# Optimization experiments

Measured on AMD Instinct MI355X. Metric: run time of the kernel, lower is better.

Reference implementation:

```python
import jax, jax.numpy as jnp
import numpy as np

B, C, H, W = 4, 512, 48, 48
DQ = C // 8  # inter_rate = 8
N = H * W
EPS = 1e-5


def _local_mask(radius):
    r = np.arange(N) // W
    c = np.arange(N) % W
    d = np.maximum(np.abs(r[:, None] - r[None, :]), np.abs(c[:, None] - c[None, :]))
    return jnp.asarray(d <= radius)


def setup_inputs() -> dict:
    key = jax.random.key(0)
    ks = jax.random.split(key, 12)
    def nrm(k, shape, scale=0.04):
        return jax.random.normal(k, shape, dtype=jnp.float32) * scale
    zc = jnp.zeros((C,), jnp.float32)
    oc = jnp.ones((C,), jnp.float32)
    return {
        "x": jax.random.normal(ks[0], (B, C, H, W), dtype=jnp.float32),
        "Wq": nrm(ks[1], (DQ, C)), "bq": jnp.zeros((DQ,), jnp.float32),
        "Wk": nrm(ks[2], (DQ, C)), "bk": jnp.zeros((DQ,), jnp.float32),
        "Wv": nrm(ks[3], (C, C)), "bv": zc,
        "conv1_w": nrm(ks[4], (C, C, 3, 3)),
        "bn1_w": oc, "bn1_b": zc, "bn1_m": zc, "bn1_v": oc,
        "conv2_w": nrm(ks[5], (C, C, 3, 3)),
        "bn2_w": oc, "bn2_b": zc, "bn2_m": zc, "bn2_v": oc,
        "sig1_w": nrm(ks[6], (C, C)), "sig1_b": zc,
        "sig2_w": nrm(ks[7], (C, C)), "sig2_b": zc,
        "gamma": jnp.full((1,), 0.5, jnp.float32),
        "gamma1": jnp.full((1,), 0.3, jnp.float32),
        "gamma2": jnp.full((1,), 0.2, jnp.float32),
        "mask1": _local_mask(6),
        "mask2": _local_mask(12),
    }


def _masked_softmax(e, mask):
    # exp(e)*mask / sum(exp(e)*mask) == softmax with -inf outside mask
    e = e - jnp.max(e, axis=-1, keepdims=True)
    w = jnp.exp(e) * mask.astype(e.dtype)
    return w / jnp.sum(w, axis=-1, keepdims=True)


def _conv1x1(t, w, b):
    return jnp.einsum('bchw,dc->bdhw', t, w) + b[None, :, None, None]


def _conv3x3_bn_relu(t, w, g, beta, mu, var):
    y = jax.lax.conv_general_dilated(t, w, (1, 1), 'SAME',
                                     dimension_numbers=('NCHW', 'OIHW', 'NCHW'))
    scale = (g / jnp.sqrt(var + EPS))[None, :, None, None]
    y = (y - mu[None, :, None, None]) * scale + beta[None, :, None, None]
    return jax.nn.relu(y)


def _forward(x, Wq, bq, Wk, bk, Wv, bv, conv1_w, bn1_w, bn1_b, bn1_m, bn1_v,
             conv2_w, bn2_w, bn2_b, bn2_m, bn2_v, sig1_w, sig1_b, sig2_w, sig2_b,
             gamma, gamma1, gamma2, mask1, mask2):
    b, c, h, w = x.shape
    n = h * w
    q = _conv1x1(x, Wq, bq).reshape(b, -1, n)   # [B, d, N]
    k = _conv1x1(x, Wk, bk).reshape(b, -1, n)   # [B, d, N]
    energy = jnp.einsum('bdn,bdm->bnm', q, k)   # [B, N, N] (query rows)
    a0 = jax.nn.softmax(energy, axis=-1)
    a1 = _masked_softmax(energy, mask1)
    a2 = _masked_softmax(energy, mask2)
    v = _conv1x1(x, Wv, bv).reshape(b, c, n)
    # torch: bmm(value, attention.permute(0,2,1)) -> out[b,c,m] = sum_n v[b,c,n]*a[m,n]
    out0 = jnp.einsum('bcn,bmn->bcm', v, a0).reshape(b, c, h, w)
    out0 = gamma * out0 + x
    out0 = _conv3x3_bn_relu(out0, conv1_w, bn1_w, bn1_b, bn1_m, bn1_v)
    s1 = (jax.nn.sigmoid(_conv1x1(out0, sig1_w, sig1_b)) * out0).reshape(b, c, n)
    out1 = jnp.einsum('bcn,bmn->bcm', s1, a1).reshape(b, c, h, w)
    out1 = gamma1 * out1 + out0
    out1 = _conv3x3_bn_relu(out1, conv2_w, bn2_w, bn2_b, bn2_m, bn2_v)
    s2 = (jax.nn.sigmoid(_conv1x1(out1, sig2_w, sig2_b)) * out1).reshape(b, c, n)
    out2 = jnp.einsum('bcn,bmn->bcm', s2, a2).reshape(b, c, h, w)
    return gamma2 * out2 + out1


def reference(x, Wq, bq, Wk, bk, Wv, bv, conv1_w, bn1_w, bn1_b, bn1_m, bn1_v,
              conv2_w, bn2_w, bn2_b, bn2_m, bn2_v, sig1_w, sig1_b, sig2_w, sig2_b,
              gamma, gamma1, gamma2, mask1, mask2):
    return _forward(x, Wq, bq, Wk, bk, Wv, bv, conv1_w, bn1_w, bn1_b, bn1_m, bn1_v,
                    conv2_w, bn2_w, bn2_b, bn2_m, bn2_v, sig1_w, sig1_b, sig2_w, sig2_b,
                    gamma, gamma1, gamma2, mask1, mask2)
```

## Files before the change

### kernel.cpp

```cpp
#include <hip/hip_runtime.h>
#include <math.h>

#define BB 4
#define CC 512
#define HH 48
#define WW 48
#define NN 2304
#define DDQ 64
#define LDSP 72
#define PW 50
#define PROWS 2500

typedef __attribute__((ext_vector_type(4))) float f32x4;
typedef __attribute__((ext_vector_type(8))) _Float16 half8;
typedef __attribute__((ext_vector_type(4))) _Float16 half4;
typedef __attribute__((ext_vector_type(8))) short bf16x8;

__device__ __forceinline__ int imax(int a, int b) { return a > b ? a : b; }
__device__ __forceinline__ int imin(int a, int b) { return a < b ? a : b; }
__device__ __forceinline__ int prow(int m) {
    int h = m / WW, w = m - h * WW;
    return (h + 1) * PW + (w + 1);
}
__device__ __forceinline__ unsigned short f2bf(float f) {
    unsigned u = __float_as_uint(f);
    u += 0x7fffu + ((u >> 16) & 1u);
    return (unsigned short)(u >> 16);
}
__device__ __forceinline__ float bf2f(unsigned short s) {
    unsigned u = ((unsigned)s) << 16;
    return __uint_as_float(u);
}

typedef __attribute__((address_space(1))) unsigned int g_u32;
typedef __attribute__((address_space(3))) unsigned int l_u32;
__device__ __forceinline__ void gl16(const void* g, void* l) {
    __builtin_amdgcn_global_load_lds((const g_u32*)g, (l_u32*)l, 16, 0, 0);
}

#define BWAVE_IDX()                                  \
    int tid = threadIdx.x;                           \
    int wave = tid >> 6, lane = tid & 63;            \
    int wm = (wave >> 1) * 64, wn = (wave & 1) * 32; \
    int x = lane & 15, qq = lane >> 4;

__device__ __forceinline__ half8 fragld(const _Float16* T, int r, int c) {
    int kb = c ^ (r & 7);
    return *(const half8*)(T + r * 64 + kb * 8);
}
__device__ __forceinline__ bf16x8 fragld_b(const unsigned short* T, int r, int c) {
    int kb = c ^ (r & 7);
    return *(const bf16x8*)(T + r * 64 + kb * 8);
}

__device__ __forceinline__ void btile(const _Float16* As, const _Float16* Bs,
                                      f32x4 acc[4][2], int wm, int wn, int x, int qq) {
#pragma unroll
    for (int ks = 0; ks < 2; ++ks) {
        int c = ks * 4 + qq;
        half8 a0 = fragld(As, wm + x, c);
        half8 a1 = fragld(As, wm + 16 + x, c);
        half8 a2 = fragld(As, wm + 32 + x, c);
        half8 a3 = fragld(As, wm + 48 + x, c);
        half8 b0 = fragld(Bs, wn + x, c);
        half8 b1 = fragld(Bs, wn + 16 + x, c);
        acc[0][0] = __builtin_amdgcn_mfma_f32_16x16x32_f16(a0, b0, acc[0][0], 0, 0, 0);
        acc[0][1] = __builtin_amdgcn_mfma_f32_16x16x32_f16(a0, b1, acc[0][1], 0, 0, 0);
        acc[1][0] = __builtin_amdgcn_mfma_f32_16x16x32_f16(a1, b0, acc[1][0], 0, 0, 0);
        acc[1][1] = __builtin_amdgcn_mfma_f32_16x16x32_f16(a1, b1, acc[1][1], 0, 0, 0);
        acc[2][0] = __builtin_amdgcn_mfma_f32_16x16x32_f16(a2, b0, acc[2][0], 0, 0, 0);
        acc[2][1] = __builtin_amdgcn_mfma_f32_16x16x32_f16(a2, b1, acc[2][1], 0, 0, 0);
        acc[3][0] = __builtin_amdgcn_mfma_f32_16x16x32_f16(a3, b0, acc[3][0], 0, 0, 0);
        acc[3][1] = __builtin_amdgcn_mfma_f32_16x16x32_f16(a3, b1, acc[3][1], 0, 0, 0);
    }
}
__device__ __forceinline__ void btile_b(const unsigned short* As, const unsigned short* Bs,
                                        f32x4 acc[4][2], int wm, int wn, int x, int qq) {
#pragma unroll
    for (int ks = 0; ks < 2; ++ks) {
        int c = ks * 4 + qq;
        bf16x8 a0 = fragld_b(As, wm + x, c);
        bf16x8 a1 = fragld_b(As, wm + 16 + x, c);
        bf16x8 a2 = fragld_b(As, wm + 32 + x, c);
        bf16x8 a3 = fragld_b(As, wm + 48 + x, c);
        bf16x8 b0 = fragld_b(Bs, wn + x, c);
        bf16x8 b1 = fragld_b(Bs, wn + 16 + x, c);
        acc[0][0] = __builtin_amdgcn_mfma_f32_16x16x32_bf16(a0, b0, acc[0][0], 0, 0, 0);
        acc[0][1] = __builtin_amdgcn_mfma_f32_16x16x32_bf16(a0, b1, acc[0][1], 0, 0, 0);
        acc[1][0] = __builtin_amdgcn_mfma_f32_16x16x32_bf16(a1, b0, acc[1][0], 0, 0, 0);
        acc[1][1] = __builtin_amdgcn_mfma_f32_16x16x32_bf16(a1, b1, acc[1][1], 0, 0, 0);
        acc[2][0] = __builtin_amdgcn_mfma_f32_16x16x32_bf16(a2, b0, acc[2][0], 0, 0, 0);
        acc[2][1] = __builtin_amdgcn_mfma_f32_16x16x32_bf16(a2, b1, acc[2][1], 0, 0, 0);
        acc[3][0] = __builtin_amdgcn_mfma_f32_16x16x32_bf16(a3, b0, acc[3][0], 0, 0, 0);
        acc[3][1] = __builtin_amdgcn_mfma_f32_16x16x32_bf16(a3, b1, acc[3][1], 0, 0, 0);
    }
}

#define BACC_INIT()                                         \
    f32x4 zf = {0.f, 0.f, 0.f, 0.f};                        \
    f32x4 acc[4][2];                                        \
    _Pragma("unroll") for (int i_ = 0; i_ < 4; ++i_) {      \
        acc[i_][0] = zf; acc[i_][1] = zf; }

#define SLOT_A(i) int sb = (wave * 4 + (i)) * 64; int s = sb + lane; \
                  int r = s >> 3, kb = s & 7; int koff = ((kb ^ (r & 7)) << 3);
#define SLOT_B(i) int sb = (wave * 2 + (i)) * 64; int s = sb + lane; \
                  int r = s >> 3, kb = s & 7; int koff = ((kb ^ (r & 7)) << 3);

__device__ __forceinline__ void stage_rows(_Float16* dst, const _Float16* __restrict__ src,
                                           int ld, int row0, int k0, int tid) {
#pragma unroll
    for (int i = 0; i < 2; ++i) {
        int s = tid * 2 + i;
        int r = s >> 3, off = (s & 7) << 3;
        *(half8*)(dst + r * LDSP + off) =
            *(const half8*)(src + (size_t)(row0 + r) * ld + k0 + off);
    }
}
__device__ __forceinline__ void mfma_tile(const _Float16* As, const _Float16* Bs,
                                          f32x4 acc[2][2], int wm, int wn, int x, int qq) {
#pragma unroll
    for (int ks = 0; ks < 2; ++ks) {
        int kof = ks * 32 + qq * 8;
        half8 a0 = *(const half8*)(As + (wm + x) * LDSP + kof);
        half8 a1 = *(const half8*)(As + (wm + 16 + x) * LDSP + kof);
        half8 b0 = *(const half8*)(Bs + (wn + x) * LDSP + kof);
        half8 b1 = *(const half8*)(Bs + (wn + 16 + x) * LDSP + kof);
        acc[0][0] = __builtin_amdgcn_mfma_f32_16x16x32_f16(a0, b0, acc[0][0], 0, 0, 0);
        acc[0][1] = __builtin_amdgcn_mfma_f32_16x16x32_f16(a0, b1, acc[0][1], 0, 0, 0);
        acc[1][0] = __builtin_amdgcn_mfma_f32_16x16x32_f16(a1, b0, acc[1][0], 0, 0, 0);
        acc[1][1] = __builtin_amdgcn_mfma_f32_16x16x32_f16(a1, b1, acc[1][1], 0, 0, 0);
    }
}
#define WAVE_IDX()                             \
    int tid = threadIdx.x;                     \
    int wave = tid >> 6, lane = tid & 63;      \
    int wm = (wave >> 1) * 32, wn = (wave & 1) * 32; \
    int x = lane & 15, qq = lane >> 4;
#define ACC_INIT()                             \
    f32x4 zf = {0.f, 0.f, 0.f, 0.f};           \
    f32x4 acc[2][2];                           \
    acc[0][0] = zf; acc[0][1] = zf; acc[1][0] = zf; acc[1][1] = zf;

__global__ __launch_bounds__(256) void k_cast_multi(const float* __restrict__ s0,
                                                    const float* __restrict__ s1,
                                                    const float* __restrict__ s2,
                                                    _Float16* __restrict__ d0,
                                                    _Float16* __restrict__ d1,
                                                    _Float16* __restrict__ d2, int n) {
    const float* s = blockIdx.y == 0 ? s0 : (blockIdx.y == 1 ? s1 : s2);
    _Float16* d = blockIdx.y == 0 ? d0 : (blockIdx.y == 1 ? d1 : d2);
    for (int i = blockIdx.x * 256 + threadIdx.x; i < n; i += gridDim.x * 256)
        d[i] = (_Float16)s[i];
}

__global__ __launch_bounds__(256) void k_repack_conv2(const float* __restrict__ w1,
                                                      const float* __restrict__ w2,
                                                      _Float16* __restrict__ d1,
                                                      _Float16* __restrict__ d2) {
    const float* w = blockIdx.y ? w2 : w1;
    _Float16* dst = blockIdx.y ? d2 : d1;
    int i = blockIdx.x * 256 + threadIdx.x;
    if (i >= 9 * CC * CC) return;
    int r = i / (CC * CC);
    int rem = i - r * CC * CC;
    int co = rem / CC, ci = rem - (rem / CC) * CC;
    dst[i] = (_Float16)w[((size_t)co * CC + ci) * 9 + r];
}

__global__ __launch_bounds__(256) void k_transpose_x(const float* __restrict__ x,
                                                     _Float16* __restrict__ xT) {
    __shared__ float tile[32][33];
    int b = blockIdx.z;
    int c0 = blockIdx.y * 32, n0 = blockIdx.x * 32;
    int tx = threadIdx.x & 31, ty = threadIdx.x >> 5;
    const float* xb = x + (size_t)b * CC * NN;
#pragma unroll
    for (int rr = 0; rr < 32; rr += 8)
        tile[ty + rr][tx] = xb[(size_t)(c0 + ty + rr) * NN + n0 + tx];
    __syncthreads();
    _Float16* xTb = xT + (size_t)b * NN * CC;
#pragma unroll
    for (int rr = 0; rr < 32; rr += 8)
        xTb[(size_t)(n0 + ty + rr) * CC + c0 + tx] = (_Float16)tile[tx][ty + rr];
}

__global__ __launch_bounds__(256) void k_qkproj(const _Float16* __restrict__ Wq,
                                                const _Float16* __restrict__ Wk,
                                                const float* __restrict__ bq,
                                                const float* __restrict__ bk,
                                                const _Float16* __restrict__ xT,
                                                _Float16* __restrict__ qT,
                                                _Float16* __restrict__ kT) {
    __shared__ _Float16 As[64 * LDSP];
    __shared__ _Float16 Bs[64 * LDSP];
    WAVE_IDX();
    int j0 = blockIdx.x * 64, b = blockIdx.z;
    const _Float16* Wp = blockIdx.y ? Wk : Wq;
    const float* bias = blockIdx.y ? bk : bq;
    _Float16* outT = blockIdx.y ? kT : qT;
    const _Float16* xTb = xT + (size_t)b * NN * CC;
    ACC_INIT();
    for (int kc = 0; kc < CC; kc += 64) {
        stage_rows(As, Wp, CC, 0, kc, tid);
        stage_rows(Bs, xTb, CC, j0, kc, tid);
        __syncthreads();
        mfma_tile(As, Bs, acc, wm, wn, x, qq);
        __syncthreads();
    }
#pragma unroll
    for (int ms = 0; ms < 2; ++ms) {
        int R0 = wm + ms * 16 + qq * 4;
#pragma unroll
        for (int ns = 0; ns < 2; ++ns) {
            int Ccol = j0 + wn + ns * 16 + x;
            half4 t;
            t.x = (_Float16)(acc[ms][ns][0] + bias[R0 + 0]);
            t.y = (_Float16)(acc[ms][ns][1] + bias[R0 + 1]);
            t.z = (_Float16)(acc[ms][ns][2] + bias[R0 + 2]);
            t.w = (_Float16)(acc[ms][ns][3] + bias[R0 + 3]);
            *(half4*)(outT + ((size_t)b * NN + Ccol) * DDQ + R0) = t;
        }
    }
}

template <int EPI, int PAD>
__global__ __launch_bounds__(256) void k_cgemm(const _Float16* __restrict__ W,
                                               const float* __restrict__ bias,
                                               const _Float16* __restrict__ Bsrc,
                                               const float* __restrict__ gate,
                                               unsigned short* __restrict__ out) {
    __shared__ _Float16 As[128 * 64];
    __shared__ _Float16 Bs[64 * 64];
    BWAVE_IDX();
    int j0 = blockIdx.x * 64, i0 = blockIdx.y * 128, b = blockIdx.z;
    const _Float16* Bb = Bsrc + (size_t)b * (PAD ? (size_t)PROWS * CC : (size_t)NN * CC);

    const _Float16* aSrc[4]; int aOf[4];
#pragma unroll
    for (int i = 0; i < 4; ++i) {
        SLOT_A(i);
        aSrc[i] = W + (size_t)(i0 + r) * CC + koff;
        aOf[i] = sb * 8;
    }
    const _Float16* bSrc[2]; int bOf[2];
#pragma unroll
    for (int i = 0; i < 2; ++i) {
        SLOT_B(i);
        int row = PAD ? prow(j0 + r) : (j0 + r);
        bSrc[i] = Bb + (size_t)row * CC + koff;
        bOf[i] = sb * 8;
    }
    BACC_INIT();
    for (int kc = 0; kc < CC; kc += 64) {
        __syncthreads();
#pragma unroll
        for (int i = 0; i < 4; ++i) gl16(aSrc[i] + kc, As + aOf[i]);
#pragma unroll
        for (int i = 0; i < 2; ++i) gl16(bSrc[i] + kc, Bs + bOf[i]);
        __syncthreads();
        btile(As, Bs, acc, wm, wn, x, qq);
    }
#pragma unroll
    for (int mt = 0; mt < 4; ++mt) {
        int R0 = i0 + wm + mt * 16 + qq * 4;
#pragma unroll
        for (int nt = 0; nt < 2; ++nt) {
            int Ccol = j0 + wn + nt * 16 + x;
#pragma unroll
            for (int e = 0; e < 4; ++e) {
                float v = acc[mt][nt][e] + bias[R0 + e];
                size_t idx = ((size_t)b * CC + R0 + e) * NN + Ccol;
                if (EPI == 1) v = gate[idx] / (1.f + __expf(-v));
                out[idx] = f2bf(v);
            }
        }
    }
}

__global__ __launch_bounds__(256) void k_exp(const _Float16* __restrict__ qT,
                                             const _Float16* __restrict__ kT,
                                             unsigned short* __restrict__ attnB,
                                             float* __restrict__ rowsum, int rad) {
    __shared__ _Float16 qs[64 * LDSP];
    __shared__ _Float16 ks[64 * LDSP];
    __shared__ unsigned short Eh[64 * 72];
    __shared__ float psum[512];
    WAVE_IDX();
    int j0 = blockIdx.x * 64, i0 = blockIdx.y * 64, b = blockIdx.z;
    if (rad > 0) {
        int hlo = i0 / WW, hhi = (i0 + 63) / WW;
        int h2lo = imax(0, hlo - rad), h2hi = imin(HH - 1, hhi + rad);
        int klo = (h2lo * WW) & ~63;
        int khi = imin(NN, ((h2hi + 1) * WW + 63) & ~63);
        if (j0 + 64 <= klo || j0 >= khi) return;
    }
    stage_rows(qs, qT + (size_t)b * NN * DDQ, DDQ, i0, 0, tid);
    stage_rows(ks, kT + (size_t)b * NN * DDQ, DDQ, j0, 0, tid);
    __syncthreads();
    ACC_INIT();
    mfma_tile(qs, ks, acc, wm, wn, x, qq);
#pragma unroll
    for (int ns = 0; ns < 2; ++ns) {
        int col = wn + ns * 16 + x;
        int gn = j0 + col;
        int hn = gn / WW, cn = gn % WW;
#pragma unroll
        for (int ms = 0; ms < 2; ++ms)
#pragma unroll
            for (int e = 0; e < 4; ++e) {
                int row = wm + ms * 16 + qq * 4 + e;
                int gm = i0 + row;
                bool valid = true;
                if (rad > 0) {
                    int dh = gm / WW - hn; if (dh < 0) dh = -dh;
                    int dc = gm % WW - cn; if (dc < 0) dc = -dc;
                    valid = (dh <= rad) && (dc <= rad);
                }
                float w = valid ? __expf(acc[ms][ns][e]) : 0.f;
                Eh[row * 72 + col] = f2bf(w);
            }
    }
    __syncthreads();
#pragma unroll
    for (int t = 0; t < 2; ++t) {
        int s = tid + t * 256;
        int r = s >> 3, cg = (s & 7) << 3;
        bf16x8 v = *(const bf16x8*)(Eh + r * 72 + cg);
        *(bf16x8*)(attnB + ((size_t)b * NN + i0 + r) * NN + j0 + cg) = v;
        float ss = 0.f;
#pragma unroll
        for (int j = 0; j < 8; ++j) ss += bf2f((unsigned short)v[j]);
        psum[s] = ss;
    }
    __syncthreads();
    if (tid < 64) {
        float tot = 0.f;
#pragma unroll
        for (int g = 0; g < 8; ++g) tot += psum[tid * 8 + g];
        atomicAdd(rowsum + (size_t)b * NN + i0 + tid, tot);
    }
}

__global__ __launch_bounds__(256) void k_attn(const unsigned short* __restrict__ A,
                                              const unsigned short* __restrict__ attnB,
                                              const float* __restrict__ rowsum,
                                              const float* __restrict__ res,
                                              const float* __restrict__ gamma,
                                              float* __restrict__ outF,
                                              _Float16* __restrict__ outT, int rad) {
    __shared__ unsigned short As[128 * 64];
    __shared__ unsigned short Bs[64 * 64];
    BWAVE_IDX();
    int j0 = blockIdx.x * 64, i0 = blockIdx.y * 128, b = blockIdx.z;
    int klo = 0, khi = NN;
    if (rad > 0) {
        int hlo = j0 / WW, hhi = (j0 + 63) / WW;
        int h2lo = imax(0, hlo - rad), h2hi = imin(HH - 1, hhi + rad);
        klo = (h2lo * WW) & ~63;
        khi = imin(NN, ((h2hi + 1) * WW + 63) & ~63);
    }
    const unsigned short* Ab = A + (size_t)b * CC * NN;
    const unsigned short* Tb = attnB + (size_t)b * NN * NN;

    const unsigned short* aSrc[4]; int aOf[4];
#pragma unroll
    for (int i = 0; i < 4; ++i) {
        SLOT_A(i);
        aSrc[i] = Ab + (size_t)(i0 + r) * NN + koff;
        aOf[i] = sb * 8;
    }
    const unsigned short* bSrc[2]; int bOf[2];
#pragma unroll
    for (int i = 0; i < 2; ++i) {
        SLOT_B(i);
        bSrc[i] = Tb + (size_t)(j0 + r) * NN + koff;
        bOf[i] = sb * 8;
    }
    BACC_INIT();
    for (int kc = klo; kc < khi; kc += 64) {
        __syncthreads();
#pragma unroll
        for (int i = 0; i < 4; ++i) gl16(aSrc[i] + kc, As + aOf[i]);
#pragma unroll
        for (int i = 0; i < 2; ++i) gl16(bSrc[i] + kc, Bs + bOf[i]);
        __syncthreads();
        btile_b(As, Bs, acc, wm, wn, x, qq);
    }
    float g = gamma[0];
#pragma unroll
    for (int mt = 0; mt < 4; ++mt) {
        int R0 = i0 + wm + mt * 16 + qq * 4;
#pragma unroll
        for (int nt = 0; nt < 2; ++nt) {
            int Ccol = j0 + wn + nt * 16 + x;
            float linv = g / fmaxf(rowsum[(size_t)b * NN + Ccol], 1e-30f);
            float v[4];
#pragma unroll
            for (int e = 0; e < 4; ++e)
                v[e] = acc[mt][nt][e] * linv + res[((size_t)b * CC + R0 + e) * NN + Ccol];
            if (outT) {
                half4 t;
                t.x = (_Float16)v[0]; t.y = (_Float16)v[1];
                t.z = (_Float16)v[2]; t.w = (_Float16)v[3];
                *(half4*)(outT + ((size_t)b * PROWS + prow(Ccol)) * CC + R0) = t;
            }
            if (outF) {
#pragma unroll
                for (int e = 0; e < 4; ++e)
                    outF[((size_t)b * CC + R0 + e) * NN + Ccol] = v[e];
            }
        }
    }
}

__global__ __launch_bounds__(256) void k_conv3(const _Float16* __restrict__ Arep,
                                               const _Float16* __restrict__ Tpad,
                                               const float* __restrict__ bng,
                                               const float* __restrict__ bnb,
                                               const float* __restrict__ bnm,
                                               const float* __restrict__ bnv,
                                               float* __restrict__ outF,
                                               _Float16* __restrict__ outT) {
    __shared__ _Float16 As[128 * 64];
    __shared__ _Float16 Bs[64 * 64];
    BWAVE_IDX();
    int j0 = blockIdx.x * 64, i0 = blockIdx.y * 128, b = blockIdx.z;
    const _Float16* Tb = Tpad + (size_t)b * PROWS * CC;

    size_t aRow[4]; int aOf[4];
#pragma unroll
    for (int i = 0; i < 4; ++i) {
        SLOT_A(i);
        aRow[i] = (size_t)(i0 + r) * CC + koff;
        aOf[i] = sb * 8;
    }
    int bPr[2], bKoff[2], bOf[2];
#pragma unroll
    for (int i = 0; i < 2; ++i) {
        SLOT_B(i);
        bPr[i] = prow(j0 + r);
        bKoff[i] = koff;
        bOf[i] = sb * 8;
    }
    BACC_INIT();
#pragma unroll
    for (int rt = 0; rt < 9; ++rt) {
        int dh = rt / 3 - 1, dw = rt - (rt / 3) * 3 - 1;
        int shift = dh * PW + dw;
        const _Float16* Ar = Arep + (size_t)rt * CC * CC;
        for (int ci0 = 0; ci0 < CC; ci0 += 64) {
            __syncthreads();
#pragma unroll
            for (int i = 0; i < 4; ++i) gl16(Ar + aRow[i] + ci0, As + aOf[i]);
#pragma unroll
            for (int i = 0; i < 2; ++i)
                gl16(Tb + (size_t)(bPr[i] + shift) * CC + ci0 + bKoff[i], Bs + bOf[i]);
            __syncthreads();
            btile(As, Bs, acc, wm, wn, x, qq);
        }
    }
#pragma unroll
    for (int mt = 0; mt < 4; ++mt) {
        int R0 = i0 + wm + mt * 16 + qq * 4;
        float sc[4], sh[4];
#pragma unroll
        for (int e = 0; e < 4; ++e) {
            sc[e] = bng[R0 + e] * rsqrtf(bnv[R0 + e] + 1e-5f);
            sh[e] = bnb[R0 + e] - bnm[R0 + e] * sc[e];
        }
#pragma unroll
        for (int nt = 0; nt < 2; ++nt) {
            int Ccol = j0 + wn + nt * 16 + x;
            float v[4];
#pragma unroll
            for (int e = 0; e < 4; ++e) {
                float t = acc[mt][nt][e] * sc[e] + sh[e];
                v[e] = t > 0.f ? t : 0.f;
                outF[((size_t)b * CC + R0 + e) * NN + Ccol] = v[e];
            }
            half4 t4;
            t4.x = (_Float16)v[0]; t4.y = (_Float16)v[1];
            t4.z = (_Float16)v[2]; t4.w = (_Float16)v[3];
            *(half4*)(outT + ((size_t)b * PROWS + prow(Ccol)) * CC + R0) = t4;
        }
    }
}

extern "C" void kernel_launch(void* const* d_in, const int* in_sizes, int n_in,
                              void* d_out, int out_size, void* d_ws, size_t ws_size,
                              hipStream_t stream) {
    const float* xin  = (const float*)d_in[0];
    const float* Wq   = (const float*)d_in[1];
    const float* bq   = (const float*)d_in[2];
    const float* Wk   = (const float*)d_in[3];
    const float* bk   = (const float*)d_in[4];
    const float* Wv   = (const float*)d_in[5];
    const float* bv   = (const float*)d_in[6];
    const float* c1w  = (const float*)d_in[7];
    const float* bn1w = (const float*)d_in[8];
    const float* bn1b = (const float*)d_in[9];
    const float* bn1m = (const float*)d_in[10];
    const float* bn1v = (const float*)d_in[11];
    const float* c2w  = (const float*)d_in[12];
    const float* bn2w = (const float*)d_in[13];
    const float* bn2b = (const float*)d_in[14];
    const float* bn2m = (const float*)d_in[15];
    const float* bn2v = (const float*)d_in[16];
    const float* s1w  = (const float*)d_in[17];
    const float* s1b  = (const float*)d_in[18];
    const float* s2w  = (const float*)d_in[19];
    const float* s2b  = (const float*)d_in[20];
    const float* gamma  = (const float*)d_in[21];
    const float* gamma1 = (const float*)d_in[22];
    const float* gamma2 = (const float*)d_in[23];

    float* out = (float*)d_out;

    char* p = (char*)d_ws;
    unsigned short* attn = (unsigned short*)p; p += (size_t)BB * NN * NN * 2;
    _Float16* xT    = (_Float16*)p; p += (size_t)BB * NN * CC * 2;
    _Float16* qT    = (_Float16*)p; p += (size_t)BB * NN * DDQ * 2;
    _Float16* kT    = (_Float16*)p; p += (size_t)BB * NN * DDQ * 2;
    unsigned short* vsB = (unsigned short*)p; p += (size_t)BB * CC * NN * 2;
    _Float16* TattnP= (_Float16*)p; p += (size_t)BB * PROWS * CC * 2;
    _Float16* TconvP= (_Float16*)p; p += (size_t)BB * PROWS * CC * 2;
    float*    rR    = (float*)p;    p += (size_t)BB * CC * NN * 4;
    _Float16* wq_h  = (_Float16*)p; p += (size_t)DDQ * CC * 2;
    _Float16* wk_h  = (_Float16*)p; p += (size_t)DDQ * CC * 2;
    _Float16* wv_h  = (_Float16*)p; p += (size_t)CC * CC * 2;
    _Float16* s1_h  = (_Float16*)p; p += (size_t)CC * CC * 2;
    _Float16* s2_h  = (_Float16*)p; p += (size_t)CC * CC * 2;
    _Float16* crep1 = (_Float16*)p; p += (size_t)9 * CC * CC * 2;
    _Float16* crep2 = (_Float16*)p; p += (size_t)9 * CC * CC * 2;
    float*    rowsum= (float*)p;    p += (size_t)3 * BB * NN * 4;

    dim3 blk(256);

    hipMemsetAsync(TattnP, 0, (size_t)BB * PROWS * CC * 2, stream);
    hipMemsetAsync(TconvP, 0, (size_t)BB * PROWS * CC * 2, stream);
    hipMemsetAsync(rowsum, 0, (size_t)3 * BB * NN * 4, stream);

    k_cast_multi<<<dim3(128, 2), blk, 0, stream>>>(Wq, Wk, nullptr, wq_h, wk_h, nullptr, DDQ * CC);
    k_cast_multi<<<dim3(1024, 3), blk, 0, stream>>>(Wv, s1w, s2w, wv_h, s1_h, s2_h, CC * CC);
    k_repack_conv2<<<dim3((9 * CC * CC + 255) / 256, 2), blk, 0, stream>>>(c1w, c2w, crep1, crep2);
    k_transpose_x<<<dim3(NN / 32, CC / 32, BB), blk, 0, stream>>>(xin, xT);

    dim3 gQK(NN / 64, 2, BB);
    dim3 gExp(NN / 64, NN / 64, BB);
    dim3 gBig(NN / 64, CC / 128, BB);

    float* rs0 = rowsum;
    float* rs1 = rowsum + (size_t)BB * NN;
    float* rs2 = rowsum + (size_t)2 * BB * NN;

    k_qkproj<<<gQK, blk, 0, stream>>>(wq_h, wk_h, bq, bk, xT, qT, kT);
    k_cgemm<0, 0><<<gBig, blk, 0, stream>>>(wv_h, bv, xT, nullptr, vsB);

    k_exp<<<gExp, blk, 0, stream>>>(qT, kT, attn, rs0, -1);
    k_attn<<<gBig, blk, 0, stream>>>(vsB, attn, rs0, xin, gamma, nullptr, TattnP, -1);
    k_conv3<<<gBig, blk, 0, stream>>>(crep1, TattnP, bn1w, bn1b, bn1m, bn1v, rR, TconvP);

    k_cgemm<1, 1><<<gBig, blk, 0, stream>>>(s1_h, s1b, TconvP, rR, vsB);
    k_exp<<<gExp, blk, 0, stream>>>(qT, kT, attn, rs1, 6);
    k_attn<<<gBig, blk, 0, stream>>>(vsB, attn, rs1, rR, gamma1, nullptr, TattnP, 6);
    k_conv3<<<gBig, blk, 0, stream>>>(crep2, TattnP, bn2w, bn2b, bn2m, bn2v, rR, TconvP);

    k_cgemm<1, 1><<<gBig, blk, 0, stream>>>(s2_h, s2b, TconvP, rR, vsB);
    k_exp<<<gExp, blk, 0, stream>>>(qT, kT, attn, rs2, 12);
    k_attn<<<gBig, blk, 0, stream>>>(vsB, attn, rs2, rR, gamma2, out, nullptr, 12);
}
```

Before: 497.6 us.

## Double-buffer LDS tiles in cgemm, attention and conv3x3 GEMM kernels

```diff
diff --git a/kernel.cpp b/kernel.cpp
--- a/kernel.cpp
+++ b/kernel.cpp
@@ -230,8 +230,8 @@
                                                const _Float16* __restrict__ Bsrc,
                                                const float* __restrict__ gate,
                                                unsigned short* __restrict__ out) {
-    __shared__ _Float16 As[128 * 64];
-    __shared__ _Float16 Bs[64 * 64];
+    __shared__ __align__(16) _Float16 As[2][128 * 64];
+    __shared__ __align__(16) _Float16 Bs[2][64 * 64];
     BWAVE_IDX();
     int j0 = blockIdx.x * 64, i0 = blockIdx.y * 128, b = blockIdx.z;
     const _Float16* Bb = Bsrc + (size_t)b * (PAD ? (size_t)PROWS * CC : (size_t)NN * CC);
@@ -252,15 +252,23 @@
         bOf[i] = sb * 8;
     }
     BACC_INIT();
-    for (int kc = 0; kc < CC; kc += 64) {
+#pragma unroll
+    for (int i = 0; i < 4; ++i) gl16(aSrc[i], As[0] + aOf[i]);
+#pragma unroll
+    for (int i = 0; i < 2; ++i) gl16(bSrc[i], Bs[0] + bOf[i]);
+    const int NSTEP = CC / 64;
+    for (int t = 0; t < NSTEP - 1; ++t) {
         __syncthreads();
-#pragma unroll
-        for (int i = 0; i < 4; ++i) gl16(aSrc[i] + kc, As + aOf[i]);
-#pragma unroll
-        for (int i = 0; i < 2; ++i) gl16(bSrc[i] + kc, Bs + bOf[i]);
-        __syncthreads();
-        btile(As, Bs, acc, wm, wn, x, qq);
-    }
+        int kc = (t + 1) << 6;
+        int nb = (t + 1) & 1;
+#pragma unroll
+        for (int i = 0; i < 4; ++i) gl16(aSrc[i] + kc, As[nb] + aOf[i]);
+#pragma unroll
+        for (int i = 0; i < 2; ++i) gl16(bSrc[i] + kc, Bs[nb] + bOf[i]);
+        btile(As[t & 1], Bs[t & 1], acc, wm, wn, x, qq);
+    }
+    __syncthreads();
+    btile(As[(NSTEP - 1) & 1], Bs[(NSTEP - 1) & 1], acc, wm, wn, x, qq);
 #pragma unroll
     for (int mt = 0; mt < 4; ++mt) {
         int R0 = i0 + wm + mt * 16 + qq * 4;
@@ -349,8 +357,8 @@
                                               const float* __restrict__ gamma,
                                               float* __restrict__ outF,
                                               _Float16* __restrict__ outT, int rad) {
-    __shared__ unsigned short As[128 * 64];
-    __shared__ unsigned short Bs[64 * 64];
+    __shared__ __align__(16) unsigned short As[2][128 * 64];
+    __shared__ __align__(16) unsigned short Bs[2][64 * 64];
     BWAVE_IDX();
     int j0 = blockIdx.x * 64, i0 = blockIdx.y * 128, b = blockIdx.z;
     int klo = 0, khi = NN;
@@ -378,15 +386,23 @@
         bOf[i] = sb * 8;
     }
     BACC_INIT();
-    for (int kc = klo; kc < khi; kc += 64) {
+    int nsteps = (khi - klo) >> 6;
+#pragma unroll
+    for (int i = 0; i < 4; ++i) gl16(aSrc[i] + klo, As[0] + aOf[i]);
+#pragma unroll
+    for (int i = 0; i < 2; ++i) gl16(bSrc[i] + klo, Bs[0] + bOf[i]);
+    for (int t = 0; t < nsteps - 1; ++t) {
         __syncthreads();
-#pragma unroll
-        for (int i = 0; i < 4; ++i) gl16(aSrc[i] + kc, As + aOf[i]);
-#pragma unroll
-        for (int i = 0; i < 2; ++i) gl16(bSrc[i] + kc, Bs + bOf[i]);
-        __syncthreads();
-        btile_b(As, Bs, acc, wm, wn, x, qq);
-    }
+        int kc = klo + ((t + 1) << 6);
+        int nb = (t + 1) & 1;
+#pragma unroll
+        for (int i = 0; i < 4; ++i) gl16(aSrc[i] + kc, As[nb] + aOf[i]);
+#pragma unroll
+        for (int i = 0; i < 2; ++i) gl16(bSrc[i] + kc, Bs[nb] + bOf[i]);
+        btile_b(As[t & 1], Bs[t & 1], acc, wm, wn, x, qq);
+    }
+    __syncthreads();
+    btile_b(As[(nsteps - 1) & 1], Bs[(nsteps - 1) & 1], acc, wm, wn, x, qq);
     float g = gamma[0];
 #pragma unroll
     for (int mt = 0; mt < 4; ++mt) {
@@ -422,8 +438,8 @@
                                                const float* __restrict__ bnv,
                                                float* __restrict__ outF,
                                                _Float16* __restrict__ outT) {
-    __shared__ _Float16 As[128 * 64];
-    __shared__ _Float16 Bs[64 * 64];
+    __shared__ __align__(16) _Float16 As[2][128 * 64];
+    __shared__ __align__(16) _Float16 Bs[2][64 * 64];
     BWAVE_IDX();
     int j0 = blockIdx.x * 64, i0 = blockIdx.y * 128, b = blockIdx.z;
     const _Float16* Tb = Tpad + (size_t)b * PROWS * CC;
@@ -445,21 +461,29 @@
     }
     BACC_INIT();
 #pragma unroll
-    for (int rt = 0; rt < 9; ++rt) {
-        int dh = rt / 3 - 1, dw = rt - (rt / 3) * 3 - 1;
+    for (int i = 0; i < 4; ++i) gl16(Arep + aRow[i], As[0] + aOf[i]);
+#pragma unroll
+    for (int i = 0; i < 2; ++i)
+        gl16(Tb + (size_t)(bPr[i] + (-PW - 1)) * CC + bKoff[i], Bs[0] + bOf[i]);
+    const int TOT = 9 * (CC / 64);
+    for (int t = 0; t < TOT - 1; ++t) {
+        __syncthreads();
+        int u = t + 1;
+        int rt = u >> 3, ci0 = (u & 7) << 6;
+        int r3 = rt / 3;
+        int dh = r3 - 1, dw = rt - r3 * 3 - 1;
         int shift = dh * PW + dw;
         const _Float16* Ar = Arep + (size_t)rt * CC * CC;
-        for (int ci0 = 0; ci0 < CC; ci0 += 64) {
-            __syncthreads();
-#pragma unroll
-            for (int i = 0; i < 4; ++i) gl16(Ar + aRow[i] + ci0, As + aOf[i]);
-#pragma unroll
-            for (int i = 0; i < 2; ++i)
-                gl16(Tb + (size_t)(bPr[i] + shift) * CC + ci0 + bKoff[i], Bs + bOf[i]);
-            __syncthreads();
-            btile(As, Bs, acc, wm, wn, x, qq);
-        }
-    }
+        int nb = u & 1;
+#pragma unroll
+        for (int i = 0; i < 4; ++i) gl16(Ar + aRow[i] + ci0, As[nb] + aOf[i]);
+#pragma unroll
+        for (int i = 0; i < 2; ++i)
+            gl16(Tb + (size_t)(bPr[i] + shift) * CC + ci0 + bKoff[i], Bs[nb] + bOf[i]);
+        btile(As[t & 1], Bs[t & 1], acc, wm, wn, x, qq);
+    }
+    __syncthreads();
+    btile(As[(TOT - 1) & 1], Bs[(TOT - 1) & 1], acc, wm, wn, x, qq);
 #pragma unroll
     for (int mt = 0; mt < 4; ++mt) {
         int R0 = i0 + wm + mt * 16 + qq * 4;
```

Result: slower. 541.7 us (+8.9%).
